# Kernel tuning notes

Measured on AMD Instinct MI355X. Metric: run time of the kernel, lower is better.

## Reference

```python
import jax, jax.numpy as jnp
import numpy as np

N_HOPS = 3
N_ENTITIES = 100000
EMB = 128
N_EDGES = 600000
N_REL = 64


def setup_inputs() -> dict:
    key = jax.random.key(0)
    k1, k2, k3, k4, k5, k6 = jax.random.split(key, 6)
    entity_emb = jax.random.normal(k1, (N_ENTITIES, EMB), dtype=jnp.float32)
    edge_emb = jax.random.normal(k2, (N_REL, EMB), dtype=jnp.float32)
    q_w = jax.random.normal(k3, (EMB, EMB), dtype=jnp.float32) * (1.0 / np.sqrt(EMB))
    k_w = jax.random.normal(k4, (EMB, EMB), dtype=jnp.float32) * (1.0 / np.sqrt(EMB))
    edge_index = jax.random.randint(k5, (2, N_EDGES), 0, N_ENTITIES, dtype=jnp.int64)
    edge_type = jax.random.randint(k6, (N_EDGES,), 0, N_REL, dtype=jnp.int64)
    return {
        "entity_emb": entity_emb,
        "edge_emb": edge_emb,
        "q_w": q_w,
        "k_w": k_w,
        "edge_index": edge_index,
        "edge_type": edge_type,
        "mess_dropout": 0,
    }


def reference(entity_emb, edge_emb, q_w, k_w, edge_index, edge_type, mess_dropout):
    head = edge_index[0]
    tail = edge_index[1]
    rel = edge_emb[edge_type]                       # [E, D] per-edge relation emb
    n = entity_emb.shape[0]

    agg = entity_emb
    out = jnp.zeros_like(entity_emb)
    for _ in range(N_HOPS):
        h = agg[head]                               # [E, D]
        t = agg[tail]                               # [E, D]
        left = h @ q_w                              # [E, D]
        right = jnp.tanh((rel * t) @ k_w)           # [E, D]
        att = jnp.sum(left * right, axis=1)         # [E]
        # scatter_softmax over destination (head) segments
        seg_max = jax.ops.segment_max(att, head, num_segments=n)
        e = jnp.exp(att - seg_max[head])
        seg_sum = jax.ops.segment_sum(e, head, num_segments=n)
        w = e / seg_sum[head]                       # [E]
        # weighted messages + scatter_mean by head
        msg = w[:, None] * rel * t                  # [E, D]
        summed = jax.ops.segment_sum(msg, head, num_segments=n)
        cnt = jax.ops.segment_sum(jnp.ones_like(att), head, num_segments=n)
        agg = summed / jnp.maximum(cnt, 1.0)[:, None]
        # mess_dropout disabled (mess_dropout == 0) -> deterministic
        # F.normalize: L2 row normalization with eps 1e-12
        norm = jnp.linalg.norm(agg, axis=1, keepdims=True)
        agg = agg / jnp.maximum(norm, 1e-12)
        out = out + agg + entity_emb
    return out
```

## Files before the change

### kernel.cpp

```cpp
#include <hip/hip_runtime.h>


#define DD 128
#define CAP1 96

typedef unsigned short u16;
typedef unsigned int u32;
typedef __attribute__((ext_vector_type(8))) __bf16 bf16x8;
typedef __attribute__((ext_vector_type(4))) float f32x4;

__device__ __forceinline__ float bf2f(u16 u) { return __uint_as_float(((u32)u) << 16); }
__device__ __forceinline__ u16 f2bf(float f) {
    u32 u = __float_as_uint(f);
    u += 0x7FFFu + ((u >> 16) & 1u);
    return (u16)(u >> 16);
}
__device__ __forceinline__ u32 cvt_pk_bf16(float a, float b) {
    u32 r;
    asm("v_cvt_pk_bf16_f32 %0, %1, %2" : "=v"(r) : "v"(a), "v"(b));
    return r;
}
__device__ __forceinline__ u32 mul_bf_bf(u32 a2, u32 b2) {
    float lo = bf2f((u16)(a2 & 0xffffu)) * bf2f((u16)(b2 & 0xffffu));
    float hi = bf2f((u16)(a2 >> 16)) * bf2f((u16)(b2 >> 16));
    return cvt_pk_bf16(lo, hi);
}
__device__ __forceinline__ float fast_tanh(float x) {
    float e = __builtin_amdgcn_exp2f(x * 2.8853900817779268f);
    float r = __builtin_amdgcn_rcpf(e + 1.f);
    return __builtin_fmaf(-2.f, r, 1.f);
}

__global__ void k_cvt(const float* __restrict__ src, u16* __restrict__ dst, int n8) {
    int i = blockIdx.x * blockDim.x + threadIdx.x;
    if (i >= n8) return;
    float4 a = ((const float4*)src)[i * 2];
    float4 b = ((const float4*)src)[i * 2 + 1];
    u32 pk[4] = {cvt_pk_bf16(a.x, a.y), cvt_pk_bf16(a.z, a.w),
                 cvt_pk_bf16(b.x, b.y), cvt_pk_bf16(b.z, b.w)};
    ((uint4*)dst)[i] = *(uint4*)pk;
}

__global__ void k_hist(const int* __restrict__ head, int E, int* __restrict__ counts) {
    int e = blockIdx.x * blockDim.x + threadIdx.x;
    if (e < E) atomicAdd(&counts[head[e]], 1);
}

__global__ void k_scan_a(const int* __restrict__ counts, int N, int* __restrict__ row_off,
                         int* __restrict__ partials) {
    __shared__ int sw[16];
    int i = blockIdx.x * 1024 + threadIdx.x;
    int v = (i < N) ? counts[i] : 0;
    int lane = threadIdx.x & 63, wid = threadIdx.x >> 6;
    int x = v;
    #pragma unroll
    for (int off = 1; off < 64; off <<= 1) {
        int t = __shfl_up(x, off);
        if (lane >= off) x += t;
    }
    if (lane == 63) sw[wid] = x;
    __syncthreads();
    if (threadIdx.x == 0) {
        int run = 0;
        for (int w0 = 0; w0 < 16; w0++) { int t = sw[w0]; sw[w0] = run; run += t; }
        partials[blockIdx.x] = run;
    }
    __syncthreads();
    if (i < N) row_off[i] = x - v + sw[wid];
}
__global__ void k_scan_b(int* __restrict__ partials, int nch) {
    if (blockIdx.x == 0 && threadIdx.x == 0) {
        int run = 0;
        for (int c = 0; c < nch; c++) { int t = partials[c]; partials[c] = run; run += t; }
    }
}
__global__ void k_scan_c(int* __restrict__ row_off, const int* __restrict__ partials, int N, int E) {
    int i = blockIdx.x * 1024 + threadIdx.x;
    if (i < N) row_off[i] += partials[blockIdx.x];
    if (i == 0) row_off[N] = E;
}
__global__ void k_fill(const int* __restrict__ head, const int* __restrict__ tail,
                       const int* __restrict__ etype, int E, const int* __restrict__ row_off,
                       int* __restrict__ cursor, int* __restrict__ c_head,
                       int* __restrict__ c_tail, int* __restrict__ c_type) {
    int e = blockIdx.x * blockDim.x + threadIdx.x;
    if (e >= E) return;
    int h = head[e];
    int p = row_off[h] + atomicAdd(&cursor[h], 1);
    c_head[p] = h; c_tail[p] = tail[e]; c_type[p] = etype[e];
}

__global__ void k_blk(const int* __restrict__ row_off, int N,
                      int* __restrict__ blk_n0, int* __restrict__ blk_n1) {
    int n = blockIdx.x * blockDim.x + threadIdx.x;
    if (n >= N) return;
    int b = row_off[n] / CAP1;
    atomicMin(&blk_n0[b], n);
    atomicMax(&blk_n1[b], n + 1);
}

__global__ void k_prep_swz(const float* __restrict__ src, u16* __restrict__ dst_swz) {
    int idx = blockIdx.x * 256 + threadIdx.x;
    if (idx >= DD * DD) return;
    int n = idx >> 7, k = idx & 127;
    float v = src[k * DD + n];
    int byte = (n * 256 + k * 2) ^ ((n & 7) << 4);
    dst_swz[byte >> 1] = f2bf(v);
}
__global__ void k_prep_plain(const float* __restrict__ src, u16* __restrict__ dst) {
    int idx = blockIdx.x * 256 + threadIdx.x;
    if (idx >= DD * DD) return;
    int n = idx >> 7, k = idx & 127;
    dst[n * DD + k] = f2bf(src[k * DD + n]);
}

__global__ void __launch_bounds__(256) k_qproj(const u16* __restrict__ aggb,
                                               const uint4* __restrict__ qwT_swz,
                                               u16* __restrict__ qh, int N) {
    __shared__ u16 sA[DD * DD];
    __shared__ u16 sB[DD * DD];
    int tid = threadIdx.x;
    {
        uint4* dst = (uint4*)sB;
        #pragma unroll
        for (int i = 0; i < 8; ++i) dst[i * 256 + tid] = qwT_swz[i * 256 + tid];
    }
    long base = (long)blockIdx.x * 128;
    int qq = tid & 3, er = tid >> 2;
    #pragma unroll
    for (int pass = 0; pass < 2; ++pass) {
        int rloc = pass * 64 + er;
        long n = base + rloc;
        int d0 = qq * 32;
        __align__(16) uint4 pk[4];
        if (n < N) {
            const uint4* ar = (const uint4*)(aggb + (size_t)n * DD + d0);
            #pragma unroll
            for (int c = 0; c < 4; ++c) pk[c] = ar[c];
        } else {
            #pragma unroll
            for (int c = 0; c < 4; ++c) pk[c] = (uint4){0u, 0u, 0u, 0u};
        }
        char* basep = (char*)sA;
        #pragma unroll
        for (int c = 0; c < 4; ++c) {
            int byte = (rloc * 256 + d0 * 2 + c * 16) ^ ((rloc & 7) << 4);
            *(uint4*)(basep + byte) = pk[c];
        }
    }
    __syncthreads();
    int lane = tid & 63, wid = tid >> 6;
    int lr = lane & 15, lg = lane >> 4;
    int rgbase = wid * 32;
    f32x4 acc[2][8];
    #pragma unroll
    for (int g = 0; g < 2; ++g)
        #pragma unroll
        for (int t = 0; t < 8; ++t) acc[g][t] = (f32x4){0.f, 0.f, 0.f, 0.f};
    const char* ab_ = (const char*)sA;
    const char* bb_ = (const char*)sB;
    int sw = (lr & 7) << 4;
    #pragma unroll
    for (int kc = 0; kc < 4; ++kc) {
        int koffb = kc * 64 + lg * 16;
        int r0 = rgbase + lr;
        bf16x8 a0 = *(const bf16x8*)(ab_ + ((r0 * 256 + koffb) ^ sw));
        bf16x8 a1 = *(const bf16x8*)(ab_ + (((r0 + 16) * 256 + koffb) ^ sw));
        #pragma unroll
        for (int t = 0; t < 8; ++t) {
            int n = t * 16 + lr;
            bf16x8 b = *(const bf16x8*)(bb_ + ((n * 256 + koffb) ^ sw));
            acc[0][t] = __builtin_amdgcn_mfma_f32_16x16x32_bf16(a0, b, acc[0][t], 0, 0, 0);
            acc[1][t] = __builtin_amdgcn_mfma_f32_16x16x32_bf16(a1, b, acc[1][t], 0, 0, 0);
        }
    }
    #pragma unroll
    for (int g = 0; g < 2; ++g)
        #pragma unroll
        for (int r = 0; r < 4; ++r) {
            long row = base + rgbase + g * 16 + lg * 4 + r;
            if (row < N) {
                u16* qrow = qh + (size_t)row * DD + lr;
                #pragma unroll
                for (int t = 0; t < 8; ++t) qrow[t * 16] = f2bf(acc[g][t][r]);
            }
        }
}

__global__ void __launch_bounds__(256, 4) k_fused(
        const u16* __restrict__ aggb, const u16* __restrict__ eembb,
        const u16* __restrict__ kwT, const u16* __restrict__ qh,
        const int* __restrict__ c_head, const int* __restrict__ c_tail,
        const int* __restrict__ c_type, const int* __restrict__ row_off,
        const int* __restrict__ blk_n0, const int* __restrict__ blk_n1,
        const float* __restrict__ entity,
        u16* __restrict__ aggb_next, float* __restrict__ outacc, int mode) {
    __shared__ u16 sX[DD * DD];
    __shared__ float satt[128];
    int n0 = blk_n0[blockIdx.x];
    if (n0 == 0x7f7f7f7f) return;
    int n1 = blk_n1[blockIdx.x];
    int p0 = row_off[n0];
    int span = min(row_off[n1] - p0, 128);
    int tid = threadIdx.x;
    int qq = tid & 3, er = tid >> 2;
    #pragma unroll
    for (int pass = 0; pass < 2; ++pass) {
        int eloc = pass * 64 + er;
        int d0 = qq * 32;
        __align__(16) u32 pk[16];
        if (eloc < span) {
            int p = p0 + eloc;
            int tl = c_tail[p], rl = c_type[p];
            const uint4* ar = (const uint4*)(aggb + (size_t)tl * DD + d0);
            const uint4* rr = (const uint4*)(eembb + (size_t)rl * DD + d0);
            #pragma unroll
            for (int c = 0; c < 4; ++c) {
                uint4 av = ar[c], rv = rr[c];
                pk[c * 4 + 0] = mul_bf_bf(av.x, rv.x);
                pk[c * 4 + 1] = mul_bf_bf(av.y, rv.y);
                pk[c * 4 + 2] = mul_bf_bf(av.z, rv.z);
                pk[c * 4 + 3] = mul_bf_bf(av.w, rv.w);
            }
        } else {
            #pragma unroll
            for (int i = 0; i < 16; ++i) pk[i] = 0u;
        }
        char* base = (char*)sX;
        #pragma unroll
        for (int c = 0; c < 4; ++c) {
            int byte = (eloc * 256 + d0 * 2 + c * 16) ^ ((eloc & 7) << 4);
            *(uint4*)(base + byte) = *(const uint4*)&pk[c * 4];
        }
    }
    __syncthreads();
    int lane = tid & 63, wid = tid >> 6;
    int lr = lane & 15, lg = lane >> 4;
    int egbase = wid * 32;
    const char* xb_ = (const char*)sX;
    int sw = (lr & 7) << 4;
    bf16x8 afrag[2][4];
    #pragma unroll
    for (int kc = 0; kc < 4; ++kc) {
        int koffb = kc * 64 + lg * 16;
        int r0 = egbase + lr;
        afrag[0][kc] = *(const bf16x8*)(xb_ + ((r0 * 256 + koffb) ^ sw));
        afrag[1][kc] = *(const bf16x8*)(xb_ + (((r0 + 16) * 256 + koffb) ^ sw));
    }
    int hh[8];
    #pragma unroll
    for (int g = 0; g < 2; ++g)
        #pragma unroll
        for (int r = 0; r < 4; ++r) {
            int eloc = egbase + g * 16 + lg * 4 + r;
            hh[g * 4 + r] = (eloc < span) ? c_head[p0 + eloc] : 0;
        }
    float attv[8] = {0.f, 0.f, 0.f, 0.f, 0.f, 0.f, 0.f, 0.f};
    #pragma unroll
    for (int t = 0; t < 8; ++t) {
        f32x4 acc0 = (f32x4){0.f, 0.f, 0.f, 0.f};
        f32x4 acc1 = (f32x4){0.f, 0.f, 0.f, 0.f};
        int n = t * 16 + lr;
        #pragma unroll
        for (int kc = 0; kc < 4; ++kc) {
            int koffe = kc * 32 + lg * 8;
            bf16x8 b = *(const bf16x8*)(kwT + n * DD + koffe);
            acc0 = __builtin_amdgcn_mfma_f32_16x16x32_bf16(afrag[0][kc], b, acc0, 0, 0, 0);
            acc1 = __builtin_amdgcn_mfma_f32_16x16x32_bf16(afrag[1][kc], b, acc1, 0, 0, 0);
        }
        #pragma unroll
        for (int r = 0; r < 4; ++r) {
            attv[r]     += fast_tanh(acc0[r]) * bf2f(qh[(size_t)hh[r] * DD + t * 16 + lr]);
            attv[4 + r] += fast_tanh(acc1[r]) * bf2f(qh[(size_t)hh[4 + r] * DD + t * 16 + lr]);
        }
    }
    #pragma unroll
    for (int off = 1; off < 16; off <<= 1) {
        #pragma unroll
        for (int i = 0; i < 8; ++i) attv[i] += __shfl_xor(attv[i], off);
    }
    if (lr == 0) {
        #pragma unroll
        for (int g = 0; g < 2; ++g)
            #pragma unroll
            for (int r = 0; r < 4; ++r) {
                int eloc = egbase + g * 16 + lg * 4 + r;
                if (eloc < span) satt[eloc] = attv[g * 4 + r];
            }
    }
    __syncthreads();
    for (int n = n0 + wid; n < n1; n += 4) {
        int s0 = row_off[n] - p0;
        int s1 = min(row_off[n + 1] - p0, 128);
        float a0 = 0.f, a1 = 0.f;
        if (s1 > s0) {
            float mv = -1e30f;
            int pp = s0 + lane;
            if (pp < s1) mv = satt[pp];
            if (pp + 64 < s1) mv = fmaxf(mv, satt[pp + 64]);
            #pragma unroll
            for (int off = 1; off < 64; off <<= 1) mv = fmaxf(mv, __shfl_xor(mv, off));
            #pragma unroll 2
            for (int p = s0; p < s1; ++p) {
                float wgt = __expf(satt[p] - mv);
                int byte = (p * 256 + lane * 4) ^ ((p & 7) << 4);
                u32 xv = *(const u32*)((const char*)sX + byte);
                a0 += wgt * bf2f((u16)(xv & 0xffffu));
                a1 += wgt * bf2f((u16)(xv >> 16));
            }
            float s = a0 * a0 + a1 * a1;
            #pragma unroll
            for (int off = 1; off < 64; off <<= 1) s += __shfl_xor(s, off);
            float sc = 1.f / fmaxf(sqrtf(s), 1e-12f);
            a0 *= sc; a1 *= sc;
        }
        size_t idx = (size_t)n * DD + lane * 2;
        *(u32*)(aggb_next + idx) = cvt_pk_bf16(a0, a1);
        float o0, o1;
        if (mode == 0) { o0 = a0; o1 = a1; }
        else { o0 = outacc[idx] + a0; o1 = outacc[idx + 1] + a1; }
        if (mode == 2) { o0 += 3.f * entity[idx]; o1 += 3.f * entity[idx + 1]; }
        outacc[idx] = o0; outacc[idx + 1] = o1;
    }
}

extern "C" void kernel_launch(void* const* d_in, const int* in_sizes, int n_in,
                              void* d_out, int out_size, void* d_ws, size_t ws_size,
                              hipStream_t stream) {
    const float* entity = (const float*)d_in[0];
    const float* eemb   = (const float*)d_in[1];
    const float* qw     = (const float*)d_in[2];
    const float* kw     = (const float*)d_in[3];
    const int*   eidx   = (const int*)d_in[4];
    const int*   etype  = (const int*)d_in[5];
    const int N = in_sizes[0] / DD;
    const int E = in_sizes[5];
    const int NREL = in_sizes[1] / DD;
    const int* head = eidx;
    const int* tail = eidx + E;
    const int NB = E / CAP1 + 2;

    char* w = (char*)d_ws;
    auto carve = [&](size_t bytes) -> void* {
        void* p = (void*)w;
        w += ((bytes + 255) / 256) * 256;
        return p;
    };
    u16* aggbA     = (u16*)carve((size_t)N * DD * 2);
    u16* aggbB     = (u16*)carve((size_t)N * DD * 2);
    u16* aggb0     = (u16*)carve((size_t)N * DD * 2);
    u16* qh        = (u16*)carve((size_t)N * DD * 2);
    u16* eembb     = (u16*)carve((size_t)NREL * DD * 2);
    int* counts    = (int*)carve((size_t)N * 4);
    int* row_off   = (int*)carve((size_t)(N + 1) * 4);
    int* cursor    = (int*)carve((size_t)N * 4);
    int* c_head    = (int*)carve((size_t)E * 4);
    int* c_tail    = (int*)carve((size_t)E * 4);
    int* c_type    = (int*)carve((size_t)E * 4);
    u16* qwT_swz   = (u16*)carve((size_t)DD * DD * 2);
    u16* kwT       = (u16*)carve((size_t)DD * DD * 2);
    int* blk_n0    = (int*)carve((size_t)NB * 4);
    int* blk_n1    = (int*)carve((size_t)NB * 4);
    int* partials  = (int*)carve(4096);
    (void)ws_size; (void)n_in; (void)out_size;

    hipMemsetAsync(counts, 0, (size_t)N * 4, stream);
    hipMemsetAsync(cursor, 0, (size_t)N * 4, stream);
    hipMemsetAsync(blk_n0, 0x7f, (size_t)NB * 4, stream);
    hipMemsetAsync(blk_n1, 0, (size_t)NB * 4, stream);
    k_prep_swz<<<(DD * DD + 255) / 256, 256, 0, stream>>>(qw, qwT_swz);
    k_prep_plain<<<(DD * DD + 255) / 256, 256, 0, stream>>>(kw, kwT);
    int n8 = N * DD / 8;
    k_cvt<<<(n8 + 255) / 256, 256, 0, stream>>>(entity, aggb0, n8);
    int r8 = NREL * DD / 8;
    k_cvt<<<(r8 + 255) / 256, 256, 0, stream>>>(eemb, eembb, r8);
    k_hist<<<(E + 255) / 256, 256, 0, stream>>>(head, E, counts);
    int nch = (N + 1023) / 1024;
    k_scan_a<<<nch, 1024, 0, stream>>>(counts, N, row_off, partials);
    k_scan_b<<<1, 64, 0, stream>>>(partials, nch);
    k_scan_c<<<nch, 1024, 0, stream>>>(row_off, partials, N, E);
    k_fill<<<(E + 255) / 256, 256, 0, stream>>>(head, tail, etype, E, row_off, cursor,
                                                c_head, c_tail, c_type);
    k_blk<<<(N + 255) / 256, 256, 0, stream>>>(row_off, N, blk_n0, blk_n1);

    const u16* cur = aggb0;
    u16* bufs[2] = {aggbA, aggbB};
    for (int hop = 0; hop < 3; hop++) {
        k_qproj<<<(N + 127) / 128, 256, 0, stream>>>(cur, (const uint4*)qwT_swz, qh, N);
        u16* nxt = bufs[hop & 1];
        int mode = (hop == 0) ? 0 : ((hop == 2) ? 2 : 1);
        k_fused<<<NB, 256, 0, stream>>>(cur, eembb, kwT, qh, c_head, c_tail, c_type,
                                        row_off, blk_n0, blk_n1, entity,
                                        nxt, (float*)d_out, mode);
        cur = nxt;
    }
}
```

Baseline: 643.4 us.

## Read Q weights from global in qproj, precompute block meta, batch gathers in fused

k_qproj stops staging the transposed Q weight matrix in LDS and reads B fragments directly from global/L2, which halves its LDS use and allows more resident blocks (launch bounds 256,4). A new k_meta kernel precomputes per-block (n0, n1, p0, span) into an int4 array, so k_fused does one load instead of a chain of dependent index loads. The gather phase in k_fused now issues all tail/type index loads and embedding loads for both passes before doing any multiply, to expose more memory-level parallelism. The cost is redundant global reads of qwT across blocks and higher register pressure from holding the loaded vectors.

```diff
diff --git a/kernel.cpp b/kernel.cpp
--- a/kernel.cpp
+++ b/kernel.cpp
@@ -98,15 +98,19 @@
     atomicMin(&blk_n0[b], n);
     atomicMax(&blk_n1[b], n + 1);
 }
-
-__global__ void k_prep_swz(const float* __restrict__ src, u16* __restrict__ dst_swz) {
-    int idx = blockIdx.x * 256 + threadIdx.x;
-    if (idx >= DD * DD) return;
-    int n = idx >> 7, k = idx & 127;
-    float v = src[k * DD + n];
-    int byte = (n * 256 + k * 2) ^ ((n & 7) << 4);
-    dst_swz[byte >> 1] = f2bf(v);
-}
+__global__ void k_meta(const int* __restrict__ blk_n0, const int* __restrict__ blk_n1,
+                       const int* __restrict__ row_off, int NB, int4* __restrict__ meta) {
+    int b = blockIdx.x * blockDim.x + threadIdx.x;
+    if (b >= NB) return;
+    int n0 = blk_n0[b];
+    if (n0 == 0x7f7f7f7f) { meta[b] = make_int4(-1, 0, 0, 0); return; }
+    int n1 = blk_n1[b];
+    int p0 = row_off[n0];
+    int span = row_off[n1] - p0;
+    if (span > 128) span = 128;
+    meta[b] = make_int4(n0, n1, p0, span);
+}
+
 __global__ void k_prep_plain(const float* __restrict__ src, u16* __restrict__ dst) {
     int idx = blockIdx.x * 256 + threadIdx.x;
     if (idx >= DD * DD) return;
@@ -114,17 +118,11 @@
     dst[n * DD + k] = f2bf(src[k * DD + n]);
 }
 
-__global__ void __launch_bounds__(256) k_qproj(const u16* __restrict__ aggb,
-                                               const uint4* __restrict__ qwT_swz,
-                                               u16* __restrict__ qh, int N) {
+__global__ void __launch_bounds__(256, 4) k_qproj(const u16* __restrict__ aggb,
+                                                  const u16* __restrict__ qwT,
+                                                  u16* __restrict__ qh, int N) {
     __shared__ u16 sA[DD * DD];
-    __shared__ u16 sB[DD * DD];
     int tid = threadIdx.x;
-    {
-        uint4* dst = (uint4*)sB;
-        #pragma unroll
-        for (int i = 0; i < 8; ++i) dst[i * 256 + tid] = qwT_swz[i * 256 + tid];
-    }
     long base = (long)blockIdx.x * 128;
     int qq = tid & 3, er = tid >> 2;
     #pragma unroll
@@ -158,18 +156,18 @@
         #pragma unroll
         for (int t = 0; t < 8; ++t) acc[g][t] = (f32x4){0.f, 0.f, 0.f, 0.f};
     const char* ab_ = (const char*)sA;
-    const char* bb_ = (const char*)sB;
     int sw = (lr & 7) << 4;
     #pragma unroll
     for (int kc = 0; kc < 4; ++kc) {
         int koffb = kc * 64 + lg * 16;
+        int koffe = kc * 32 + lg * 8;
         int r0 = rgbase + lr;
         bf16x8 a0 = *(const bf16x8*)(ab_ + ((r0 * 256 + koffb) ^ sw));
         bf16x8 a1 = *(const bf16x8*)(ab_ + (((r0 + 16) * 256 + koffb) ^ sw));
         #pragma unroll
         for (int t = 0; t < 8; ++t) {
             int n = t * 16 + lr;
-            bf16x8 b = *(const bf16x8*)(bb_ + ((n * 256 + koffb) ^ sw));
+            bf16x8 b = *(const bf16x8*)(qwT + n * DD + koffe);
             acc[0][t] = __builtin_amdgcn_mfma_f32_16x16x32_bf16(a0, b, acc[0][t], 0, 0, 0);
             acc[1][t] = __builtin_amdgcn_mfma_f32_16x16x32_bf16(a1, b, acc[1][t], 0, 0, 0);
         }
@@ -192,45 +190,54 @@
         const u16* __restrict__ kwT, const u16* __restrict__ qh,
         const int* __restrict__ c_head, const int* __restrict__ c_tail,
         const int* __restrict__ c_type, const int* __restrict__ row_off,
-        const int* __restrict__ blk_n0, const int* __restrict__ blk_n1,
-        const float* __restrict__ entity,
-        u16* __restrict__ aggb_next, float* __restrict__ outacc, int mode) {
+        const int4* __restrict__ meta, const float* __restrict__ entity,
+        u16* __restrict__ aggb_next, float* __restrict__ outacc, int mode, int E) {
     __shared__ u16 sX[DD * DD];
     __shared__ float satt[128];
-    int n0 = blk_n0[blockIdx.x];
-    if (n0 == 0x7f7f7f7f) return;
-    int n1 = blk_n1[blockIdx.x];
-    int p0 = row_off[n0];
-    int span = min(row_off[n1] - p0, 128);
+    int4 mt = meta[blockIdx.x];
+    if (mt.x < 0) return;
+    int n0 = mt.x, n1 = mt.y, p0 = mt.z, span = mt.w;
     int tid = threadIdx.x;
     int qq = tid & 3, er = tid >> 2;
-    #pragma unroll
-    for (int pass = 0; pass < 2; ++pass) {
-        int eloc = pass * 64 + er;
-        int d0 = qq * 32;
-        __align__(16) u32 pk[16];
-        if (eloc < span) {
+    int d0 = qq * 32;
+    {
+        int tl[2], rl[2];
+        bool valid[2];
+        #pragma unroll
+        for (int pass = 0; pass < 2; ++pass) {
+            int eloc = pass * 64 + er;
+            valid[pass] = (eloc < span);
             int p = p0 + eloc;
-            int tl = c_tail[p], rl = c_type[p];
-            const uint4* ar = (const uint4*)(aggb + (size_t)tl * DD + d0);
-            const uint4* rr = (const uint4*)(eembb + (size_t)rl * DD + d0);
+            if (p >= E) p = E - 1;
+            tl[pass] = c_tail[p];
+            rl[pass] = c_type[p];
+        }
+        uint4 av[2][4], rv[2][4];
+        #pragma unroll
+        for (int pass = 0; pass < 2; ++pass) {
+            const uint4* ar = (const uint4*)(aggb + (size_t)tl[pass] * DD + d0);
+            const uint4* rr = (const uint4*)(eembb + (size_t)rl[pass] * DD + d0);
+            #pragma unroll
+            for (int c = 0; c < 4; ++c) { av[pass][c] = ar[c]; rv[pass][c] = rr[c]; }
+        }
+        char* base = (char*)sX;
+        #pragma unroll
+        for (int pass = 0; pass < 2; ++pass) {
+            int eloc = pass * 64 + er;
+            __align__(16) u32 pk[4];
             #pragma unroll
             for (int c = 0; c < 4; ++c) {
-                uint4 av = ar[c], rv = rr[c];
-                pk[c * 4 + 0] = mul_bf_bf(av.x, rv.x);
-                pk[c * 4 + 1] = mul_bf_bf(av.y, rv.y);
-                pk[c * 4 + 2] = mul_bf_bf(av.z, rv.z);
-                pk[c * 4 + 3] = mul_bf_bf(av.w, rv.w);
+                if (valid[pass]) {
+                    pk[0] = mul_bf_bf(av[pass][c].x, rv[pass][c].x);
+                    pk[1] = mul_bf_bf(av[pass][c].y, rv[pass][c].y);
+                    pk[2] = mul_bf_bf(av[pass][c].z, rv[pass][c].z);
+                    pk[3] = mul_bf_bf(av[pass][c].w, rv[pass][c].w);
+                } else {
+                    pk[0] = pk[1] = pk[2] = pk[3] = 0u;
+                }
+                int byte = (eloc * 256 + d0 * 2 + c * 16) ^ ((eloc & 7) << 4);
+                *(uint4*)(base + byte) = *(const uint4*)pk;
             }
-        } else {
-            #pragma unroll
-            for (int i = 0; i < 16; ++i) pk[i] = 0u;
-        }
-        char* base = (char*)sX;
-        #pragma unroll
-        for (int c = 0; c < 4; ++c) {
-            int byte = (eloc * 256 + d0 * 2 + c * 16) ^ ((eloc & 7) << 4);
-            *(uint4*)(base + byte) = *(const uint4*)&pk[c * 4];
         }
     }
     __syncthreads();
@@ -357,10 +364,11 @@
     int* c_head    = (int*)carve((size_t)E * 4);
     int* c_tail    = (int*)carve((size_t)E * 4);
     int* c_type    = (int*)carve((size_t)E * 4);
-    u16* qwT_swz   = (u16*)carve((size_t)DD * DD * 2);
+    u16* qwT       = (u16*)carve((size_t)DD * DD * 2);
     u16* kwT       = (u16*)carve((size_t)DD * DD * 2);
     int* blk_n0    = (int*)carve((size_t)NB * 4);
     int* blk_n1    = (int*)carve((size_t)NB * 4);
+    int4* meta     = (int4*)carve((size_t)NB * 16);
     int* partials  = (int*)carve(4096);
     (void)ws_size; (void)n_in; (void)out_size;
 
@@ -368,7 +376,7 @@
     hipMemsetAsync(cursor, 0, (size_t)N * 4, stream);
     hipMemsetAsync(blk_n0, 0x7f, (size_t)NB * 4, stream);
     hipMemsetAsync(blk_n1, 0, (size_t)NB * 4, stream);
-    k_prep_swz<<<(DD * DD + 255) / 256, 256, 0, stream>>>(qw, qwT_swz);
+    k_prep_plain<<<(DD * DD + 255) / 256, 256, 0, stream>>>(qw, qwT);
     k_prep_plain<<<(DD * DD + 255) / 256, 256, 0, stream>>>(kw, kwT);
     int n8 = N * DD / 8;
     k_cvt<<<(n8 + 255) / 256, 256, 0, stream>>>(entity, aggb0, n8);
@@ -382,16 +390,17 @@
     k_fill<<<(E + 255) / 256, 256, 0, stream>>>(head, tail, etype, E, row_off, cursor,
                                                 c_head, c_tail, c_type);
     k_blk<<<(N + 255) / 256, 256, 0, stream>>>(row_off, N, blk_n0, blk_n1);
+    k_meta<<<(NB + 255) / 256, 256, 0, stream>>>(blk_n0, blk_n1, row_off, NB, meta);
 
     const u16* cur = aggb0;
     u16* bufs[2] = {aggbA, aggbB};
     for (int hop = 0; hop < 3; hop++) {
-        k_qproj<<<(N + 127) / 128, 256, 0, stream>>>(cur, (const uint4*)qwT_swz, qh, N);
+        k_qproj<<<(N + 127) / 128, 256, 0, stream>>>(cur, qwT, qh, N);
         u16* nxt = bufs[hop & 1];
         int mode = (hop == 0) ? 0 : ((hop == 2) ? 2 : 1);
         k_fused<<<NB, 256, 0, stream>>>(cur, eembb, kwT, qh, c_head, c_tail, c_type,
-                                        row_off, blk_n0, blk_n1, entity,
-                                        nxt, (float*)d_out, mode);
+                                        row_off, meta, entity,
+                                        nxt, (float*)d_out, mode, E);
         cur = nxt;
     }
 }
```

Result: slower. 672.2 us (+4.5%).

## Make fused hop kernel persistent with prefetch of next block's gathered rows

Applied to the files above, without the earlier changes.

The fused attention/aggregation kernel becomes a grid-stride persistent kernel capped at 1024 blocks. While the current block runs its MFMA and softmax, it prefetches the next block's tail-row gathers into registers. A new metadata kernel packs n0, n1, p0 and span per block into an int4 so each block needs one load instead of several dependent ones. The aim is to hide gather latency and cut block launch overhead, at the cost of more registers (two sets of eight uint4 prefetch buffers), which could lower occupancy under launch_bounds(256,4).

```diff
diff --git a/kernel.cpp b/kernel.cpp
--- a/kernel.cpp
+++ b/kernel.cpp
@@ -98,6 +98,18 @@
     atomicMin(&blk_n0[b], n);
     atomicMax(&blk_n1[b], n + 1);
 }
+__global__ void k_meta(const int* __restrict__ blk_n0, const int* __restrict__ blk_n1,
+                       const int* __restrict__ row_off, int NB, int4* __restrict__ meta) {
+    int b = blockIdx.x * blockDim.x + threadIdx.x;
+    if (b >= NB) return;
+    int n0 = blk_n0[b];
+    if (n0 == 0x7f7f7f7f) { meta[b] = make_int4(-1, 0, 0, 0); return; }
+    int n1 = blk_n1[b];
+    int p0 = row_off[n0];
+    int span = row_off[n1] - p0;
+    if (span > 128) span = 128;
+    meta[b] = make_int4(n0, n1, p0, span);
+}
 
 __global__ void k_prep_swz(const float* __restrict__ src, u16* __restrict__ dst_swz) {
     int idx = blockIdx.x * 256 + threadIdx.x;
@@ -192,135 +204,185 @@
         const u16* __restrict__ kwT, const u16* __restrict__ qh,
         const int* __restrict__ c_head, const int* __restrict__ c_tail,
         const int* __restrict__ c_type, const int* __restrict__ row_off,
-        const int* __restrict__ blk_n0, const int* __restrict__ blk_n1,
-        const float* __restrict__ entity,
-        u16* __restrict__ aggb_next, float* __restrict__ outacc, int mode) {
+        const int4* __restrict__ meta, const float* __restrict__ entity,
+        u16* __restrict__ aggb_next, float* __restrict__ outacc,
+        int mode, int NB, int E) {
     __shared__ u16 sX[DD * DD];
     __shared__ float satt[128];
-    int n0 = blk_n0[blockIdx.x];
-    if (n0 == 0x7f7f7f7f) return;
-    int n1 = blk_n1[blockIdx.x];
-    int p0 = row_off[n0];
-    int span = min(row_off[n1] - p0, 128);
     int tid = threadIdx.x;
     int qq = tid & 3, er = tid >> 2;
-    #pragma unroll
-    for (int pass = 0; pass < 2; ++pass) {
-        int eloc = pass * 64 + er;
-        int d0 = qq * 32;
-        __align__(16) u32 pk[16];
-        if (eloc < span) {
-            int p = p0 + eloc;
-            int tl = c_tail[p], rl = c_type[p];
-            const uint4* ar = (const uint4*)(aggb + (size_t)tl * DD + d0);
-            const uint4* rr = (const uint4*)(eembb + (size_t)rl * DD + d0);
-            #pragma unroll
-            for (int c = 0; c < 4; ++c) {
-                uint4 av = ar[c], rv = rr[c];
-                pk[c * 4 + 0] = mul_bf_bf(av.x, rv.x);
-                pk[c * 4 + 1] = mul_bf_bf(av.y, rv.y);
-                pk[c * 4 + 2] = mul_bf_bf(av.z, rv.z);
-                pk[c * 4 + 3] = mul_bf_bf(av.w, rv.w);
-            }
-        } else {
-            #pragma unroll
-            for (int i = 0; i < 16; ++i) pk[i] = 0u;
-        }
-        char* base = (char*)sX;
-        #pragma unroll
-        for (int c = 0; c < 4; ++c) {
-            int byte = (eloc * 256 + d0 * 2 + c * 16) ^ ((eloc & 7) << 4);
-            *(uint4*)(base + byte) = *(const uint4*)&pk[c * 4];
-        }
-    }
-    __syncthreads();
+    int d0 = qq * 32;
     int lane = tid & 63, wid = tid >> 6;
     int lr = lane & 15, lg = lane >> 4;
-    int egbase = wid * 32;
-    const char* xb_ = (const char*)sX;
     int sw = (lr & 7) << 4;
-    bf16x8 afrag[2][4];
-    #pragma unroll
-    for (int kc = 0; kc < 4; ++kc) {
-        int koffb = kc * 64 + lg * 16;
-        int r0 = egbase + lr;
-        afrag[0][kc] = *(const bf16x8*)(xb_ + ((r0 * 256 + koffb) ^ sw));
-        afrag[1][kc] = *(const bf16x8*)(xb_ + (((r0 + 16) * 256 + koffb) ^ sw));
-    }
-    int hh[8];
-    #pragma unroll
-    for (int g = 0; g < 2; ++g)
-        #pragma unroll
-        for (int r = 0; r < 4; ++r) {
-            int eloc = egbase + g * 16 + lg * 4 + r;
-            hh[g * 4 + r] = (eloc < span) ? c_head[p0 + eloc] : 0;
-        }
-    float attv[8] = {0.f, 0.f, 0.f, 0.f, 0.f, 0.f, 0.f, 0.f};
-    #pragma unroll
-    for (int t = 0; t < 8; ++t) {
-        f32x4 acc0 = (f32x4){0.f, 0.f, 0.f, 0.f};
-        f32x4 acc1 = (f32x4){0.f, 0.f, 0.f, 0.f};
-        int n = t * 16 + lr;
-        #pragma unroll
-        for (int kc = 0; kc < 4; ++kc) {
-            int koffe = kc * 32 + lg * 8;
-            bf16x8 b = *(const bf16x8*)(kwT + n * DD + koffe);
-            acc0 = __builtin_amdgcn_mfma_f32_16x16x32_bf16(afrag[0][kc], b, acc0, 0, 0, 0);
-            acc1 = __builtin_amdgcn_mfma_f32_16x16x32_bf16(afrag[1][kc], b, acc1, 0, 0, 0);
-        }
-        #pragma unroll
-        for (int r = 0; r < 4; ++r) {
-            attv[r]     += fast_tanh(acc0[r]) * bf2f(qh[(size_t)hh[r] * DD + t * 16 + lr]);
-            attv[4 + r] += fast_tanh(acc1[r]) * bf2f(qh[(size_t)hh[4 + r] * DD + t * 16 + lr]);
-        }
-    }
-    #pragma unroll
-    for (int off = 1; off < 16; off <<= 1) {
-        #pragma unroll
-        for (int i = 0; i < 8; ++i) attv[i] += __shfl_xor(attv[i], off);
-    }
-    if (lr == 0) {
-        #pragma unroll
-        for (int g = 0; g < 2; ++g)
-            #pragma unroll
-            for (int r = 0; r < 4; ++r) {
-                int eloc = egbase + g * 16 + lg * 4 + r;
-                if (eloc < span) satt[eloc] = attv[g * 4 + r];
-            }
-    }
-    __syncthreads();
-    for (int n = n0 + wid; n < n1; n += 4) {
-        int s0 = row_off[n] - p0;
-        int s1 = min(row_off[n + 1] - p0, 128);
-        float a0 = 0.f, a1 = 0.f;
-        if (s1 > s0) {
-            float mv = -1e30f;
-            int pp = s0 + lane;
-            if (pp < s1) mv = satt[pp];
-            if (pp + 64 < s1) mv = fmaxf(mv, satt[pp + 64]);
-            #pragma unroll
-            for (int off = 1; off < 64; off <<= 1) mv = fmaxf(mv, __shfl_xor(mv, off));
-            #pragma unroll 2
-            for (int p = s0; p < s1; ++p) {
-                float wgt = __expf(satt[p] - mv);
-                int byte = (p * 256 + lane * 4) ^ ((p & 7) << 4);
-                u32 xv = *(const u32*)((const char*)sX + byte);
-                a0 += wgt * bf2f((u16)(xv & 0xffffu));
-                a1 += wgt * bf2f((u16)(xv >> 16));
-            }
-            float s = a0 * a0 + a1 * a1;
-            #pragma unroll
-            for (int off = 1; off < 64; off <<= 1) s += __shfl_xor(s, off);
-            float sc = 1.f / fmaxf(sqrtf(s), 1e-12f);
-            a0 *= sc; a1 *= sc;
-        }
-        size_t idx = (size_t)n * DD + lane * 2;
-        *(u32*)(aggb_next + idx) = cvt_pk_bf16(a0, a1);
-        float o0, o1;
-        if (mode == 0) { o0 = a0; o1 = a1; }
-        else { o0 = outacc[idx] + a0; o1 = outacc[idx + 1] + a1; }
-        if (mode == 2) { o0 += 3.f * entity[idx]; o1 += 3.f * entity[idx + 1]; }
-        outacc[idx] = o0; outacc[idx + 1] = o1;
+
+    int b = blockIdx.x;
+    if (b >= NB) return;
+    int4 mt = meta[b];
+    uint4 av0[4], av1[4];
+    int rl0 = 0, rl1 = 0;
+    bool v0 = false, v1 = false;
+    {
+        int p0 = mt.z, span = mt.w;
+        v0 = (mt.x >= 0) && (er < span);
+        v1 = (mt.x >= 0) && (64 + er < span);
+        int pp0 = min(v0 ? p0 + er : p0, E - 1);
+        int pp1 = min(v1 ? p0 + 64 + er : p0, E - 1);
+        int t0 = c_tail[pp0], t1 = c_tail[pp1];
+        rl0 = c_type[pp0]; rl1 = c_type[pp1];
+        const uint4* ar0 = (const uint4*)(aggb + (size_t)t0 * DD + d0);
+        const uint4* ar1 = (const uint4*)(aggb + (size_t)t1 * DD + d0);
+        #pragma unroll
+        for (int c = 0; c < 4; ++c) { av0[c] = ar0[c]; av1[c] = ar1[c]; }
+    }
+    for (;;) {
+        if (mt.x >= 0) {
+            const uint4* rr0 = (const uint4*)(eembb + (size_t)rl0 * DD + d0);
+            const uint4* rr1 = (const uint4*)(eembb + (size_t)rl1 * DD + d0);
+            char* base = (char*)sX;
+            #pragma unroll
+            for (int c = 0; c < 4; ++c) {
+                uint4 rv = rr0[c];
+                __align__(16) u32 pk[4];
+                if (v0) {
+                    pk[0] = mul_bf_bf(av0[c].x, rv.x);
+                    pk[1] = mul_bf_bf(av0[c].y, rv.y);
+                    pk[2] = mul_bf_bf(av0[c].z, rv.z);
+                    pk[3] = mul_bf_bf(av0[c].w, rv.w);
+                } else { pk[0] = pk[1] = pk[2] = pk[3] = 0u; }
+                int byte = (er * 256 + d0 * 2 + c * 16) ^ ((er & 7) << 4);
+                *(uint4*)(base + byte) = *(const uint4*)pk;
+            }
+            int e1 = 64 + er;
+            #pragma unroll
+            for (int c = 0; c < 4; ++c) {
+                uint4 rv = rr1[c];
+                __align__(16) u32 pk[4];
+                if (v1) {
+                    pk[0] = mul_bf_bf(av1[c].x, rv.x);
+                    pk[1] = mul_bf_bf(av1[c].y, rv.y);
+                    pk[2] = mul_bf_bf(av1[c].z, rv.z);
+                    pk[3] = mul_bf_bf(av1[c].w, rv.w);
+                } else { pk[0] = pk[1] = pk[2] = pk[3] = 0u; }
+                int byte = (e1 * 256 + d0 * 2 + c * 16) ^ ((e1 & 7) << 4);
+                *(uint4*)(base + byte) = *(const uint4*)pk;
+            }
+        }
+        __syncthreads();
+        int bn = b + gridDim.x;
+        bool have_next = (bn < NB);
+        int4 mtn = make_int4(-1, 0, 0, 0);
+        uint4 nav0[4], nav1[4];
+        int nrl0 = 0, nrl1 = 0;
+        bool nv0 = false, nv1 = false;
+        if (have_next) {
+            mtn = meta[bn];
+            int p0 = mtn.z, span = mtn.w;
+            nv0 = (mtn.x >= 0) && (er < span);
+            nv1 = (mtn.x >= 0) && (64 + er < span);
+            int pp0 = min(nv0 ? p0 + er : p0, E - 1);
+            int pp1 = min(nv1 ? p0 + 64 + er : p0, E - 1);
+            int t0 = c_tail[pp0], t1 = c_tail[pp1];
+            nrl0 = c_type[pp0]; nrl1 = c_type[pp1];
+            const uint4* ar0 = (const uint4*)(aggb + (size_t)t0 * DD + d0);
+            const uint4* ar1 = (const uint4*)(aggb + (size_t)t1 * DD + d0);
+            #pragma unroll
+            for (int c = 0; c < 4; ++c) { nav0[c] = ar0[c]; nav1[c] = ar1[c]; }
+        }
+        if (mt.x >= 0) {
+            int n0 = mt.x, n1 = mt.y, p0 = mt.z, span = mt.w;
+            const char* xb_ = (const char*)sX;
+            int egbase = wid * 32;
+            bf16x8 afrag[2][4];
+            #pragma unroll
+            for (int kc = 0; kc < 4; ++kc) {
+                int koffb = kc * 64 + lg * 16;
+                int r0 = egbase + lr;
+                afrag[0][kc] = *(const bf16x8*)(xb_ + ((r0 * 256 + koffb) ^ sw));
+                afrag[1][kc] = *(const bf16x8*)(xb_ + (((r0 + 16) * 256 + koffb) ^ sw));
+            }
+            int hh[8];
+            #pragma unroll
+            for (int g = 0; g < 2; ++g)
+                #pragma unroll
+                for (int r = 0; r < 4; ++r) {
+                    int eloc = egbase + g * 16 + lg * 4 + r;
+                    hh[g * 4 + r] = (eloc < span) ? c_head[p0 + eloc] : 0;
+                }
+            float attv[8] = {0.f, 0.f, 0.f, 0.f, 0.f, 0.f, 0.f, 0.f};
+            #pragma unroll
+            for (int t = 0; t < 8; ++t) {
+                f32x4 acc0 = (f32x4){0.f, 0.f, 0.f, 0.f};
+                f32x4 acc1 = (f32x4){0.f, 0.f, 0.f, 0.f};
+                int n = t * 16 + lr;
+                #pragma unroll
+                for (int kc = 0; kc < 4; ++kc) {
+                    int koffe = kc * 32 + lg * 8;
+                    bf16x8 bb = *(const bf16x8*)(kwT + n * DD + koffe);
+                    acc0 = __builtin_amdgcn_mfma_f32_16x16x32_bf16(afrag[0][kc], bb, acc0, 0, 0, 0);
+                    acc1 = __builtin_amdgcn_mfma_f32_16x16x32_bf16(afrag[1][kc], bb, acc1, 0, 0, 0);
+                }
+                #pragma unroll
+                for (int r = 0; r < 4; ++r) {
+                    attv[r]     += fast_tanh(acc0[r]) * bf2f(qh[(size_t)hh[r] * DD + t * 16 + lr]);
+                    attv[4 + r] += fast_tanh(acc1[r]) * bf2f(qh[(size_t)hh[4 + r] * DD + t * 16 + lr]);
+                }
+            }
+            #pragma unroll
+            for (int off = 1; off < 16; off <<= 1) {
+                #pragma unroll
+                for (int i = 0; i < 8; ++i) attv[i] += __shfl_xor(attv[i], off);
+            }
+            if (lr == 0) {
+                #pragma unroll
+                for (int g = 0; g < 2; ++g)
+                    #pragma unroll
+                    for (int r = 0; r < 4; ++r) {
+                        int eloc = egbase + g * 16 + lg * 4 + r;
+                        if (eloc < span) satt[eloc] = attv[g * 4 + r];
+                    }
+            }
+            __syncthreads();
+            for (int n = n0 + wid; n < n1; n += 4) {
+                int s0 = row_off[n] - p0;
+                int s1 = min(row_off[n + 1] - p0, 128);
+                float a0 = 0.f, a1 = 0.f;
+                if (s1 > s0) {
+                    float mv = -1e30f;
+                    int pp = s0 + lane;
+                    if (pp < s1) mv = satt[pp];
+                    if (pp + 64 < s1) mv = fmaxf(mv, satt[pp + 64]);
+                    #pragma unroll
+                    for (int off = 1; off < 64; off <<= 1) mv = fmaxf(mv, __shfl_xor(mv, off));
+                    #pragma unroll 2
+                    for (int p = s0; p < s1; ++p) {
+                        float wgt = __expf(satt[p] - mv);
+                        int byte = (p * 256 + lane * 4) ^ ((p & 7) << 4);
+                        u32 xv = *(const u32*)((const char*)sX + byte);
+                        a0 += wgt * bf2f((u16)(xv & 0xffffu));
+                        a1 += wgt * bf2f((u16)(xv >> 16));
+                    }
+                    float s = a0 * a0 + a1 * a1;
+                    #pragma unroll
+                    for (int off = 1; off < 64; off <<= 1) s += __shfl_xor(s, off);
+                    float sc = 1.f / fmaxf(sqrtf(s), 1e-12f);
+                    a0 *= sc; a1 *= sc;
+                }
+                size_t idx = (size_t)n * DD + lane * 2;
+                *(u32*)(aggb_next + idx) = cvt_pk_bf16(a0, a1);
+                float o0, o1;
+                if (mode == 0) { o0 = a0; o1 = a1; }
+                else { o0 = outacc[idx] + a0; o1 = outacc[idx + 1] + a1; }
+                if (mode == 2) { o0 += 3.f * entity[idx]; o1 += 3.f * entity[idx + 1]; }
+                outacc[idx] = o0; outacc[idx + 1] = o1;
+            }
+        }
+        __syncthreads();
+        if (!have_next) break;
+        b = bn; mt = mtn;
+        #pragma unroll
+        for (int c = 0; c < 4; ++c) { av0[c] = nav0[c]; av1[c] = nav1[c]; }
+        rl0 = nrl0; rl1 = nrl1; v0 = nv0; v1 = nv1;
     }
 }
 
@@ -361,6 +423,7 @@
     u16* kwT       = (u16*)carve((size_t)DD * DD * 2);
     int* blk_n0    = (int*)carve((size_t)NB * 4);
     int* blk_n1    = (int*)carve((size_t)NB * 4);
+    int4* meta     = (int4*)carve((size_t)NB * 16);
     int* partials  = (int*)carve(4096);
     (void)ws_size; (void)n_in; (void)out_size;
 
@@ -382,16 +445,18 @@
     k_fill<<<(E + 255) / 256, 256, 0, stream>>>(head, tail, etype, E, row_off, cursor,
                                                 c_head, c_tail, c_type);
     k_blk<<<(N + 255) / 256, 256, 0, stream>>>(row_off, N, blk_n0, blk_n1);
-
+    k_meta<<<(NB + 255) / 256, 256, 0, stream>>>(blk_n0, blk_n1, row_off, NB, meta);
+
+    int grid = NB < 1024 ? NB : 1024;
     const u16* cur = aggb0;
     u16* bufs[2] = {aggbA, aggbB};
     for (int hop = 0; hop < 3; hop++) {
         k_qproj<<<(N + 127) / 128, 256, 0, stream>>>(cur, (const uint4*)qwT_swz, qh, N);
         u16* nxt = bufs[hop & 1];
         int mode = (hop == 0) ? 0 : ((hop == 2) ? 2 : 1);
-        k_fused<<<NB, 256, 0, stream>>>(cur, eembb, kwT, qh, c_head, c_tail, c_type,
-                                        row_off, blk_n0, blk_n1, entity,
-                                        nxt, (float*)d_out, mode);
+        k_fused<<<grid, 256, 0, stream>>>(cur, eembb, kwT, qh, c_head, c_tail, c_type,
+                                          row_off, meta, entity,
+                                          nxt, (float*)d_out, mode, NB, E);
         cur = nxt;
     }
 }
```

After: 1.263 ms. 96.3% more time.
